# Kernel tuning notes

Hardware: AMD Instinct MI355X
Metric: run time of the kernel (lower is better)

The kernel has to match this reference:

```python
import jax, jax.numpy as jnp
import numpy as np

N = 100000
E = 1600000
IN_DIM = 64
OUT_DIM = 64


def setup_inputs() -> dict:
    key = jax.random.key(0)
    ks = jax.random.split(key, 10)
    q = jax.random.normal(ks[0], (N, IN_DIM), dtype=jnp.float32)
    src1 = jax.random.randint(ks[1], (E,), 0, N, dtype=jnp.int32)
    dst1 = jax.random.randint(ks[2], (E,), 0, N, dtype=jnp.int32)
    src2 = jax.random.randint(ks[3], (E,), 0, N, dtype=jnp.int32)
    dst2 = jax.random.randint(ks[4], (E,), 0, N, dtype=jnp.int32)
    # Learned parameters (torch nn.Linear default-ish init scale)
    s_att = 1.0 / np.sqrt(2 * IN_DIM)
    s_lin = 1.0 / np.sqrt(IN_DIM)
    W_att = jax.random.uniform(ks[5], (2 * IN_DIM,), jnp.float32, -s_att, s_att)  # fc_att weight [1, 2*in_dim] flattened
    W_upd = jax.random.uniform(ks[6], (OUT_DIM, IN_DIM), jnp.float32, -s_lin, s_lin)
    W_V = jax.random.uniform(ks[7], (OUT_DIM, IN_DIM), jnp.float32, -s_lin, s_lin)
    b_V = jax.random.uniform(ks[8], (OUT_DIM,), jnp.float32, -s_lin, s_lin)
    return {"q": q, "W_att": W_att, "W_upd": W_upd, "W_V": W_V, "b_V": b_V,
            "src1": src1, "dst1": dst1, "src2": src2, "dst2": dst2}


def _gat_etype(q, src, dst, W_att, W_V, b_V):
    """One edge-type pass: edge gather -> sigmoid att -> segment softmax over dst -> weighted scatter-sum."""
    d = q.shape[1]
    # fc_att(cat[q_src, q_dst]) == q_src @ W_att[:d] + q_dst @ W_att[d:] (no cat materialized)
    att_src = q @ W_att[:d]           # [N]
    att_dst = q @ W_att[d:]           # [N]
    e = jax.nn.sigmoid(att_src[src] + att_dst[dst])  # [E], in (0,1) so exp is safe without max-shift
    ex = jnp.exp(e)
    denom = jax.ops.segment_sum(ex, dst, num_segments=q.shape[0])  # [N]
    a = ex / jnp.maximum(denom[dst], 1e-12)                        # segment softmax, [E]
    qs = q[src]                                                    # [E, d] edge gather
    OK = jax.ops.segment_sum(a[:, None] * qs, dst, num_segments=q.shape[0])          # [N, d]
    V = qs @ W_V.T + b_V                                                              # [E, out]
    OV = jax.ops.segment_sum(a[:, None] * V, dst, num_segments=q.shape[0])            # [N, out]
    return OK, OV


def reference(q, W_att, W_upd, W_V, b_V, src1, dst1, src2, dst2):
    OK1, OV1 = _gat_etype(q, src1, dst1, W_att, W_V, b_V)
    OK2, OV2 = _gat_etype(q, src2, dst2, W_att, W_V, b_V)
    # multi_update_all cross-reducer 'sum': per-etype reduce (incl. fc_upd) then sum
    q_new = (q + OK1) @ W_upd.T + (q + OK2) @ W_upd.T
    OV = OV1 + OV2
    return q_new, OV
```

## Files before the change

kernel.cpp:

```cpp
#include <hip/hip_runtime.h>
#include <math.h>

#define N_NODES 100000
#define N_EDGES 1600000
#define TWO_E   (2 * N_EDGES)
#define DIM 64
#define SCAN_BLOCKS 98

__device__ __forceinline__ float edge_ex(float as, float ad) {
    float x = as + ad;
    float sg = 1.0f / (1.0f + __expf(-x));
    return __expf(sg);
}

__global__ __launch_bounds__(256) void att_kernel(const float* __restrict__ q,
                                                  const float* __restrict__ W_att,
                                                  float* __restrict__ att_src,
                                                  float* __restrict__ att_dst) {
    int wave = (blockIdx.x * blockDim.x + threadIdx.x) >> 6;
    int lane = threadIdx.x & 63;
    if (wave >= N_NODES) return;
    float qv = q[wave * DIM + lane];
    float ps = qv * W_att[lane];
    float pd = qv * W_att[DIM + lane];
    #pragma unroll
    for (int off = 32; off >= 1; off >>= 1) {
        ps += __shfl_xor(ps, off);
        pd += __shfl_xor(pd, off);
    }
    if (lane == 0) {
        att_src[wave] = ps;
        att_dst[wave] = pd;
    }
}

__global__ __launch_bounds__(256) void hist_kernel(const int* __restrict__ dst1,
                                                   const int* __restrict__ dst2,
                                                   int* __restrict__ count,
                                                   int* __restrict__ rank) {
    int idx = blockIdx.x * blockDim.x + threadIdx.x;
    if (idx >= TWO_E) return;
    int d = (idx < N_EDGES) ? dst1[idx] : dst2[idx - N_EDGES];
    rank[idx] = atomicAdd(count + d, 1);
}

__global__ __launch_bounds__(1024) void scan1_kernel(const int* __restrict__ count,
                                                     int* __restrict__ offsets,
                                                     int* __restrict__ bsum) {
    __shared__ int wtot[16];
    int i = blockIdx.x * 1024 + threadIdx.x;
    int v = (i < N_NODES) ? count[i] : 0;
    int lane = threadIdx.x & 63, wid = threadIdx.x >> 6;
    int x = v;
    #pragma unroll
    for (int off = 1; off <= 32; off <<= 1) {
        int y = __shfl_up(x, off);
        if (lane >= off) x += y;
    }
    if (lane == 63) wtot[wid] = x;
    __syncthreads();
    if (threadIdx.x < 16) {
        int t = wtot[threadIdx.x];
        #pragma unroll
        for (int off = 1; off <= 8; off <<= 1) {
            int y = __shfl_up(t, off);
            if (threadIdx.x >= off) t += y;
        }
        wtot[threadIdx.x] = t;
    }
    __syncthreads();
    int woff = (wid == 0) ? 0 : wtot[wid - 1];
    if (i < N_NODES) offsets[i] = woff + x - v;
    if (threadIdx.x == 0) bsum[blockIdx.x] = wtot[15];
}

__global__ __launch_bounds__(128) void scan2_kernel(const int* __restrict__ bsum,
                                                    int* __restrict__ boff) {
    __shared__ int s[SCAN_BLOCKS];
    if (threadIdx.x < SCAN_BLOCKS) s[threadIdx.x] = bsum[threadIdx.x];
    __syncthreads();
    if (threadIdx.x == 0) {
        int run = 0;
        for (int b = 0; b < SCAN_BLOCKS; ++b) { int t = s[b]; s[b] = run; run += t; }
    }
    __syncthreads();
    if (threadIdx.x < SCAN_BLOCKS) boff[threadIdx.x] = s[threadIdx.x];
}

__global__ __launch_bounds__(1024) void scan3_kernel(int* __restrict__ offsets,
                                                     const int* __restrict__ boff) {
    int i = blockIdx.x * 1024 + threadIdx.x;
    if (i < N_NODES) offsets[i] += boff[blockIdx.x];
    if (i == N_NODES - 1) offsets[N_NODES] = TWO_E;
}

__global__ __launch_bounds__(256) void scatter_kernel(const int* __restrict__ src1, const int* __restrict__ dst1,
                                                      const int* __restrict__ src2, const int* __restrict__ dst2,
                                                      const float* __restrict__ att_src, const float* __restrict__ att_dst,
                                                      const int* __restrict__ offsets, const int* __restrict__ rank,
                                                      uint2* __restrict__ recs) {
    int idx = blockIdx.x * blockDim.x + threadIdx.x;
    if (idx >= TWO_E) return;
    int s, d; unsigned tb;
    if (idx < N_EDGES) { s = src1[idx]; d = dst1[idx]; tb = 0u; }
    else               { s = src2[idx - N_EDGES]; d = dst2[idx - N_EDGES]; tb = 0x80000000u; }
    float ex = edge_ex(att_src[s], att_dst[d]);
    int pos = offsets[d] + rank[idx];
    recs[pos] = make_uint2((unsigned)s | tb, __float_as_uint(ex));
}

__global__ __launch_bounds__(256) void gather_kernel(const float* __restrict__ q,
                                                     const int* __restrict__ offsets,
                                                     const uint2* __restrict__ recs,
                                                     float* __restrict__ S,
                                                     float* __restrict__ fbuf) {
    int node = blockIdx.x * 16 + (threadIdx.x >> 4);
    int t = threadIdx.x & 15;
    if (node >= N_NODES) return;
    int beg = offsets[node], end = offsets[node + 1];
    float d1 = 0.f, d2 = 0.f;
    for (int i = beg + t; i < end; i += 16) {
        uint2 r = recs[i];
        float ex = __uint_as_float(r.y);
        if ((int)r.x < 0) d2 += ex; else d1 += ex;
    }
    #pragma unroll
    for (int off = 8; off >= 1; off >>= 1) {
        d1 += __shfl_xor(d1, off);
        d2 += __shfl_xor(d2, off);
    }
    float inv1 = (d1 > 0.f) ? (1.0f / d1) : 0.f;
    float inv2 = (d2 > 0.f) ? (1.0f / d2) : 0.f;
    if (t == 0) fbuf[node] = ((d1 > 0.f) ? 1.f : 0.f) + ((d2 > 0.f) ? 1.f : 0.f);

    float4 acc = make_float4(0.f, 0.f, 0.f, 0.f);
    const float* qb = q + t * 4;
    int i = beg;
    for (; i + 1 < end; i += 2) {
        uint2 r0 = recs[i], r1 = recs[i + 1];
        int s0 = r0.x & 0x7fffffff, s1 = r1.x & 0x7fffffff;
        float a0 = __uint_as_float(r0.y) * (((int)r0.x < 0) ? inv2 : inv1);
        float a1 = __uint_as_float(r1.y) * (((int)r1.x < 0) ? inv2 : inv1);
        const float4 q0 = *reinterpret_cast<const float4*>(qb + (size_t)s0 * DIM);
        const float4 q1 = *reinterpret_cast<const float4*>(qb + (size_t)s1 * DIM);
        acc.x += a0 * q0.x; acc.y += a0 * q0.y; acc.z += a0 * q0.z; acc.w += a0 * q0.w;
        acc.x += a1 * q1.x; acc.y += a1 * q1.y; acc.z += a1 * q1.z; acc.w += a1 * q1.w;
    }
    if (i < end) {
        uint2 r = recs[i];
        int s = r.x & 0x7fffffff;
        float a = __uint_as_float(r.y) * (((int)r.x < 0) ? inv2 : inv1);
        const float4 qv = *reinterpret_cast<const float4*>(qb + (size_t)s * DIM);
        acc.x += a * qv.x; acc.y += a * qv.y; acc.z += a * qv.z; acc.w += a * qv.w;
    }
    *reinterpret_cast<float4*>(S + (size_t)node * DIM + t * 4) = acc;
}

__global__ __launch_bounds__(512) void final_kernel(const float* __restrict__ q,
                                                    const float* __restrict__ W_upd,
                                                    const float* __restrict__ W_V,
                                                    const float* __restrict__ b_V,
                                                    const float* __restrict__ fbuf,
                                                    float* __restrict__ q_new,
                                                    float* S_and_OV) {
    int lane = threadIdx.x & 63;
    int w = threadIdx.x >> 6;
    int ms = __builtin_amdgcn_readfirstlane(w >> 2);
    int cs = __builtin_amdgcn_readfirstlane(w & 3);
    int node = blockIdx.x * 64 + lane;
    bool active = node < N_NODES;

    float r[DIM];
    float f = 0.f;
    if (active) {
        const float* srow = S_and_OV + (size_t)node * DIM;
        if (ms == 0) {
            #pragma unroll
            for (int k = 0; k < 16; ++k) {
                float4 v = *reinterpret_cast<const float4*>(srow + 4 * k);
                r[4 * k + 0] = v.x; r[4 * k + 1] = v.y;
                r[4 * k + 2] = v.z; r[4 * k + 3] = v.w;
            }
            f = fbuf[node];
        } else {
            const float* qrow = q + (size_t)node * DIM;
            #pragma unroll
            for (int k = 0; k < 16; ++k) {
                float4 sv = *reinterpret_cast<const float4*>(srow + 4 * k);
                float4 qv = *reinterpret_cast<const float4*>(qrow + 4 * k);
                r[4 * k + 0] = 2.f * qv.x + sv.x;
                r[4 * k + 1] = 2.f * qv.y + sv.y;
                r[4 * k + 2] = 2.f * qv.z + sv.z;
                r[4 * k + 3] = 2.f * qv.w + sv.w;
            }
        }
    } else {
        #pragma unroll
        for (int d = 0; d < DIM; ++d) r[d] = 0.f;
    }

    __syncthreads();

    const float* Wbase = ms ? W_upd : W_V;
    float acc[16];
    #pragma unroll
    for (int j = 0; j < 16; ++j) acc[j] = (ms == 0) ? f * b_V[cs * 16 + j] : 0.f;
    #pragma unroll
    for (int j = 0; j < 16; ++j) {
        const float* wr = Wbase + (cs * 16 + j) * DIM;
        float a = acc[j];
        #pragma unroll
        for (int d = 0; d < DIM; ++d) a += r[d] * wr[d];
        acc[j] = a;
    }

    if (active) {
        float* outp = (ms ? q_new : S_and_OV) + (size_t)node * DIM + cs * 16;
        #pragma unroll
        for (int k = 0; k < 4; ++k)
            *reinterpret_cast<float4*>(outp + 4 * k) =
                make_float4(acc[4 * k], acc[4 * k + 1], acc[4 * k + 2], acc[4 * k + 3]);
    }
}

extern "C" void kernel_launch(void* const* d_in, const int* in_sizes, int n_in,
                              void* d_out, int out_size, void* d_ws, size_t ws_size,
                              hipStream_t stream) {
    const float* q     = (const float*)d_in[0];
    const float* W_att = (const float*)d_in[1];
    const float* W_upd = (const float*)d_in[2];
    const float* W_V   = (const float*)d_in[3];
    const float* b_V   = (const float*)d_in[4];
    const int*   src1  = (const int*)d_in[5];
    const int*   dst1  = (const int*)d_in[6];
    const int*   src2  = (const int*)d_in[7];
    const int*   dst2  = (const int*)d_in[8];

    float* out   = (float*)d_out;
    float* q_new = out;
    float* S     = out + (size_t)N_NODES * DIM;
    uint2* recs  = (uint2*)q_new;

    float* att_src = (float*)d_ws;
    float* att_dst = att_src + N_NODES;
    float* fbuf    = att_dst + N_NODES;
    int*   count   = (int*)(fbuf + N_NODES);
    int*   offsets = count + N_NODES;
    int*   bsum    = offsets + N_NODES + 1;
    int*   boff    = bsum + 128;
    int*   rank    = boff + 128;

    hipMemsetAsync(count, 0, (size_t)N_NODES * sizeof(int), stream);

    att_kernel<<<N_NODES / 4, 256, 0, stream>>>(q, W_att, att_src, att_dst);
    hist_kernel<<<(TWO_E + 255) / 256, 256, 0, stream>>>(dst1, dst2, count, rank);
    scan1_kernel<<<SCAN_BLOCKS, 1024, 0, stream>>>(count, offsets, bsum);
    scan2_kernel<<<1, 128, 0, stream>>>(bsum, boff);
    scan3_kernel<<<SCAN_BLOCKS, 1024, 0, stream>>>(offsets, boff);
    scatter_kernel<<<(TWO_E + 255) / 256, 256, 0, stream>>>(
        src1, dst1, src2, dst2, att_src, att_dst, offsets, rank, recs);
    gather_kernel<<<(N_NODES + 15) / 16, 256, 0, stream>>>(q, offsets, recs, S, fbuf);
    final_kernel<<<(N_NODES + 63) / 64, 512, 0, stream>>>(
        q, W_upd, W_V, b_V, fbuf, q_new, S);
}
```

Baseline: 577.2 us.

## Replace per-node CSR sort with coarse 64-node bucket sort and in-LDS regroup

```diff
diff --git a/kernel.cpp b/kernel.cpp
--- a/kernel.cpp
+++ b/kernel.cpp
@@ -5,7 +5,10 @@
 #define N_EDGES 1600000
 #define TWO_E   (2 * N_EDGES)
 #define DIM 64
-#define SCAN_BLOCKS 98
+#define NB 1563
+#define EPB 16384
+#define HS_BLOCKS ((TWO_E + EPB - 1) / EPB)
+#define CAP 2048
 
 __device__ __forceinline__ float edge_ex(float as, float ad) {
     float x = as + ad;
@@ -34,126 +37,168 @@
     }
 }
 
-__global__ __launch_bounds__(256) void hist_kernel(const int* __restrict__ dst1,
-                                                   const int* __restrict__ dst2,
-                                                   int* __restrict__ count,
-                                                   int* __restrict__ rank) {
-    int idx = blockIdx.x * blockDim.x + threadIdx.x;
-    if (idx >= TWO_E) return;
-    int d = (idx < N_EDGES) ? dst1[idx] : dst2[idx - N_EDGES];
-    rank[idx] = atomicAdd(count + d, 1);
-}
-
-__global__ __launch_bounds__(1024) void scan1_kernel(const int* __restrict__ count,
-                                                     int* __restrict__ offsets,
-                                                     int* __restrict__ bsum) {
-    __shared__ int wtot[16];
-    int i = blockIdx.x * 1024 + threadIdx.x;
-    int v = (i < N_NODES) ? count[i] : 0;
-    int lane = threadIdx.x & 63, wid = threadIdx.x >> 6;
-    int x = v;
+__global__ __launch_bounds__(1024) void hist_coarse(const int* __restrict__ dst1,
+                                                    const int* __restrict__ dst2,
+                                                    int* __restrict__ bcount) {
+    __shared__ int lh[NB];
+    for (int b = threadIdx.x; b < NB; b += 1024) lh[b] = 0;
+    __syncthreads();
+    int base = blockIdx.x * EPB;
+    int lim = min(base + EPB, TWO_E);
+    for (int idx = base + threadIdx.x; idx < lim; idx += 1024) {
+        int d = (idx < N_EDGES) ? dst1[idx] : dst2[idx - N_EDGES];
+        atomicAdd(&lh[d >> 6], 1);
+    }
+    __syncthreads();
+    for (int b = threadIdx.x; b < NB; b += 1024)
+        if (lh[b]) atomicAdd(bcount + b, lh[b]);
+}
+
+__global__ __launch_bounds__(1024) void scan_coarse(const int* __restrict__ bcount,
+                                                    int* __restrict__ bbase,
+                                                    int* __restrict__ bcursor) {
+    __shared__ int wt[16];
+    int t = threadIdx.x;
+    int i0 = 2 * t, i1 = 2 * t + 1;
+    int v0 = (i0 < NB) ? bcount[i0] : 0;
+    int v1 = (i1 < NB) ? bcount[i1] : 0;
+    int p = v0 + v1;
+    int lane = t & 63, wid = t >> 6;
+    int x = p;
     #pragma unroll
     for (int off = 1; off <= 32; off <<= 1) {
         int y = __shfl_up(x, off);
         if (lane >= off) x += y;
     }
-    if (lane == 63) wtot[wid] = x;
-    __syncthreads();
-    if (threadIdx.x < 16) {
-        int t = wtot[threadIdx.x];
+    if (lane == 63) wt[wid] = x;
+    __syncthreads();
+    if (t < 16) {
+        int s = wt[t];
         #pragma unroll
         for (int off = 1; off <= 8; off <<= 1) {
-            int y = __shfl_up(t, off);
-            if (threadIdx.x >= off) t += y;
-        }
-        wtot[threadIdx.x] = t;
-    }
-    __syncthreads();
-    int woff = (wid == 0) ? 0 : wtot[wid - 1];
-    if (i < N_NODES) offsets[i] = woff + x - v;
-    if (threadIdx.x == 0) bsum[blockIdx.x] = wtot[15];
-}
-
-__global__ __launch_bounds__(128) void scan2_kernel(const int* __restrict__ bsum,
-                                                    int* __restrict__ boff) {
-    __shared__ int s[SCAN_BLOCKS];
-    if (threadIdx.x < SCAN_BLOCKS) s[threadIdx.x] = bsum[threadIdx.x];
-    __syncthreads();
-    if (threadIdx.x == 0) {
-        int run = 0;
-        for (int b = 0; b < SCAN_BLOCKS; ++b) { int t = s[b]; s[b] = run; run += t; }
-    }
-    __syncthreads();
-    if (threadIdx.x < SCAN_BLOCKS) boff[threadIdx.x] = s[threadIdx.x];
-}
-
-__global__ __launch_bounds__(1024) void scan3_kernel(int* __restrict__ offsets,
-                                                     const int* __restrict__ boff) {
-    int i = blockIdx.x * 1024 + threadIdx.x;
-    if (i < N_NODES) offsets[i] += boff[blockIdx.x];
-    if (i == N_NODES - 1) offsets[N_NODES] = TWO_E;
-}
-
-__global__ __launch_bounds__(256) void scatter_kernel(const int* __restrict__ src1, const int* __restrict__ dst1,
-                                                      const int* __restrict__ src2, const int* __restrict__ dst2,
-                                                      const float* __restrict__ att_src, const float* __restrict__ att_dst,
-                                                      const int* __restrict__ offsets, const int* __restrict__ rank,
-                                                      uint2* __restrict__ recs) {
-    int idx = blockIdx.x * blockDim.x + threadIdx.x;
-    if (idx >= TWO_E) return;
-    int s, d; unsigned tb;
-    if (idx < N_EDGES) { s = src1[idx]; d = dst1[idx]; tb = 0u; }
-    else               { s = src2[idx - N_EDGES]; d = dst2[idx - N_EDGES]; tb = 0x80000000u; }
-    float ex = edge_ex(att_src[s], att_dst[d]);
-    int pos = offsets[d] + rank[idx];
-    recs[pos] = make_uint2((unsigned)s | tb, __float_as_uint(ex));
-}
-
-__global__ __launch_bounds__(256) void gather_kernel(const float* __restrict__ q,
-                                                     const int* __restrict__ offsets,
-                                                     const uint2* __restrict__ recs,
-                                                     float* __restrict__ S,
-                                                     float* __restrict__ fbuf) {
-    int node = blockIdx.x * 16 + (threadIdx.x >> 4);
-    int t = threadIdx.x & 15;
-    if (node >= N_NODES) return;
-    int beg = offsets[node], end = offsets[node + 1];
+            int y = __shfl_up(s, off);
+            if (t >= off) s += y;
+        }
+        wt[t] = s;
+    }
+    __syncthreads();
+    int pre = ((wid ? wt[wid - 1] : 0)) + (x - p);
+    if (i0 < NB) { bbase[i0] = pre;      bcursor[i0] = pre; }
+    if (i1 < NB) { bbase[i1] = pre + v0; bcursor[i1] = pre + v0; }
+    if (t == 0) bbase[NB] = wt[15];
+}
+
+__global__ __launch_bounds__(1024) void scatter_coarse(const int* __restrict__ src1, const int* __restrict__ dst1,
+                                                       const int* __restrict__ src2, const int* __restrict__ dst2,
+                                                       const float* __restrict__ att_src, const float* __restrict__ att_dst,
+                                                       int* __restrict__ bcursor,
+                                                       uint2* __restrict__ recs) {
+    __shared__ int lh[NB];
+    __shared__ int gb[NB];
+    __shared__ int lc[NB];
+    for (int b = threadIdx.x; b < NB; b += 1024) lh[b] = 0;
+    __syncthreads();
+    int base = blockIdx.x * EPB;
+    int lim = min(base + EPB, TWO_E);
+    for (int idx = base + threadIdx.x; idx < lim; idx += 1024) {
+        int d = (idx < N_EDGES) ? dst1[idx] : dst2[idx - N_EDGES];
+        atomicAdd(&lh[d >> 6], 1);
+    }
+    __syncthreads();
+    for (int b = threadIdx.x; b < NB; b += 1024) {
+        int c = lh[b];
+        lc[b] = 0;
+        gb[b] = c ? atomicAdd(bcursor + b, c) : 0;
+    }
+    __syncthreads();
+    for (int idx = base + threadIdx.x; idx < lim; idx += 1024) {
+        int s, d; unsigned ty;
+        if (idx < N_EDGES) { s = src1[idx]; d = dst1[idx]; ty = 0u; }
+        else               { s = src2[idx - N_EDGES]; d = dst2[idx - N_EDGES]; ty = 1u; }
+        int b = d >> 6;
+        int r = atomicAdd(&lc[b], 1);
+        float ex = edge_ex(att_src[s], att_dst[d]);
+        recs[gb[b] + r] = make_uint2((unsigned)s | (ty << 17) | ((unsigned)(d & 63) << 18),
+                                     __float_as_uint(ex));
+    }
+}
+
+__global__ __launch_bounds__(1024) void gather_coarse(const float* __restrict__ q,
+                                                      const int* __restrict__ bbase,
+                                                      const uint2* __restrict__ recs,
+                                                      float* __restrict__ S,
+                                                      float* __restrict__ fbuf) {
+    __shared__ uint2 srt[CAP];
+    __shared__ int cnt[64];
+    __shared__ int cb[64];
+    int tid = threadIdx.x;
+    int bkt = blockIdx.x;
+    int beg = bbase[bkt], end = bbase[bkt + 1];
+    int g = tid >> 4, t16 = tid & 15;
+
+    float4 acc1 = make_float4(0.f, 0.f, 0.f, 0.f);
+    float4 acc2 = make_float4(0.f, 0.f, 0.f, 0.f);
     float d1 = 0.f, d2 = 0.f;
-    for (int i = beg + t; i < end; i += 16) {
-        uint2 r = recs[i];
-        float ex = __uint_as_float(r.y);
-        if ((int)r.x < 0) d2 += ex; else d1 += ex;
-    }
-    #pragma unroll
-    for (int off = 8; off >= 1; off >>= 1) {
-        d1 += __shfl_xor(d1, off);
-        d2 += __shfl_xor(d2, off);
-    }
-    float inv1 = (d1 > 0.f) ? (1.0f / d1) : 0.f;
-    float inv2 = (d2 > 0.f) ? (1.0f / d2) : 0.f;
-    if (t == 0) fbuf[node] = ((d1 > 0.f) ? 1.f : 0.f) + ((d2 > 0.f) ? 1.f : 0.f);
-
-    float4 acc = make_float4(0.f, 0.f, 0.f, 0.f);
-    const float* qb = q + t * 4;
-    int i = beg;
-    for (; i + 1 < end; i += 2) {
-        uint2 r0 = recs[i], r1 = recs[i + 1];
-        int s0 = r0.x & 0x7fffffff, s1 = r1.x & 0x7fffffff;
-        float a0 = __uint_as_float(r0.y) * (((int)r0.x < 0) ? inv2 : inv1);
-        float a1 = __uint_as_float(r1.y) * (((int)r1.x < 0) ? inv2 : inv1);
-        const float4 q0 = *reinterpret_cast<const float4*>(qb + (size_t)s0 * DIM);
-        const float4 q1 = *reinterpret_cast<const float4*>(qb + (size_t)s1 * DIM);
-        acc.x += a0 * q0.x; acc.y += a0 * q0.y; acc.z += a0 * q0.z; acc.w += a0 * q0.w;
-        acc.x += a1 * q1.x; acc.y += a1 * q1.y; acc.z += a1 * q1.z; acc.w += a1 * q1.w;
-    }
-    if (i < end) {
-        uint2 r = recs[i];
-        int s = r.x & 0x7fffffff;
-        float a = __uint_as_float(r.y) * (((int)r.x < 0) ? inv2 : inv1);
-        const float4 qv = *reinterpret_cast<const float4*>(qb + (size_t)s * DIM);
-        acc.x += a * qv.x; acc.y += a * qv.y; acc.z += a * qv.z; acc.w += a * qv.w;
-    }
-    *reinterpret_cast<float4*>(S + (size_t)node * DIM + t * 4) = acc;
+
+    for (int cbeg = beg; cbeg < end; cbeg += CAP) {
+        int C = min(CAP, end - cbeg);
+        __syncthreads();
+        if (tid < 64) cnt[tid] = 0;
+        __syncthreads();
+        uint2 r0, r1; int n0 = -1, n1 = -1, rk0 = 0, rk1 = 0;
+        if (tid < C) {
+            r0 = recs[cbeg + tid];
+            n0 = (r0.x >> 18) & 63;
+            rk0 = atomicAdd(&cnt[n0], 1);
+        }
+        if (tid + 1024 < C) {
+            r1 = recs[cbeg + tid + 1024];
+            n1 = (r1.x >> 18) & 63;
+            rk1 = atomicAdd(&cnt[n1], 1);
+        }
+        __syncthreads();
+        if (tid < 64) {
+            int c = cnt[tid];
+            int incl = c;
+            #pragma unroll
+            for (int off = 1; off <= 32; off <<= 1) {
+                int y = __shfl_up(incl, off);
+                if (tid >= off) incl += y;
+            }
+            cb[tid] = incl - c;
+        }
+        __syncthreads();
+        if (n0 >= 0) srt[cb[n0] + rk0] = r0;
+        if (n1 >= 0) srt[cb[n1] + rk1] = r1;
+        __syncthreads();
+        int s0 = cb[g], e0 = s0 + cnt[g];
+        for (int k = s0; k < e0; ++k) {
+            uint2 r = srt[k];
+            int s = r.x & 0x1FFFF;
+            float exv = __uint_as_float(r.y);
+            int ty = (r.x >> 17) & 1;
+            float w1 = ty ? 0.f : exv;
+            float w2 = ty ? exv : 0.f;
+            d1 += w1; d2 += w2;
+            const float4 qv = *reinterpret_cast<const float4*>(q + (size_t)s * DIM + t16 * 4);
+            acc1.x += w1 * qv.x; acc1.y += w1 * qv.y; acc1.z += w1 * qv.z; acc1.w += w1 * qv.w;
+            acc2.x += w2 * qv.x; acc2.y += w2 * qv.y; acc2.z += w2 * qv.z; acc2.w += w2 * qv.w;
+        }
+    }
+
+    float inv1 = (d1 > 0.f) ? 1.0f / d1 : 0.f;
+    float inv2 = (d2 > 0.f) ? 1.0f / d2 : 0.f;
+    int node = bkt * 64 + g;
+    if (node < N_NODES) {
+        float4 sv;
+        sv.x = acc1.x * inv1 + acc2.x * inv2;
+        sv.y = acc1.y * inv1 + acc2.y * inv2;
+        sv.z = acc1.z * inv1 + acc2.z * inv2;
+        sv.w = acc1.w * inv1 + acc2.w * inv2;
+        *reinterpret_cast<float4*>(S + (size_t)node * DIM + t16 * 4) = sv;
+        if (t16 == 0)
+            fbuf[node] = ((d1 > 0.f) ? 1.f : 0.f) + ((d2 > 0.f) ? 1.f : 0.f);
+    }
 }
 
 __global__ __launch_bounds__(512) void final_kernel(const float* __restrict__ q,
@@ -244,22 +289,18 @@
     float* att_src = (float*)d_ws;
     float* att_dst = att_src + N_NODES;
     float* fbuf    = att_dst + N_NODES;
-    int*   count   = (int*)(fbuf + N_NODES);
-    int*   offsets = count + N_NODES;
-    int*   bsum    = offsets + N_NODES + 1;
-    int*   boff    = bsum + 128;
-    int*   rank    = boff + 128;
-
-    hipMemsetAsync(count, 0, (size_t)N_NODES * sizeof(int), stream);
+    int*   bcount  = (int*)(fbuf + N_NODES);
+    int*   bbase   = bcount + NB;
+    int*   bcursor = bbase + NB + 1;
+
+    hipMemsetAsync(bcount, 0, NB * sizeof(int), stream);
 
     att_kernel<<<N_NODES / 4, 256, 0, stream>>>(q, W_att, att_src, att_dst);
-    hist_kernel<<<(TWO_E + 255) / 256, 256, 0, stream>>>(dst1, dst2, count, rank);
-    scan1_kernel<<<SCAN_BLOCKS, 1024, 0, stream>>>(count, offsets, bsum);
-    scan2_kernel<<<1, 128, 0, stream>>>(bsum, boff);
-    scan3_kernel<<<SCAN_BLOCKS, 1024, 0, stream>>>(offsets, boff);
-    scatter_kernel<<<(TWO_E + 255) / 256, 256, 0, stream>>>(
-        src1, dst1, src2, dst2, att_src, att_dst, offsets, rank, recs);
-    gather_kernel<<<(N_NODES + 15) / 16, 256, 0, stream>>>(q, offsets, recs, S, fbuf);
+    hist_coarse<<<HS_BLOCKS, 1024, 0, stream>>>(dst1, dst2, bcount);
+    scan_coarse<<<1, 1024, 0, stream>>>(bcount, bbase, bcursor);
+    scatter_coarse<<<HS_BLOCKS, 1024, 0, stream>>>(
+        src1, dst1, src2, dst2, att_src, att_dst, bcursor, recs);
+    gather_coarse<<<NB, 1024, 0, stream>>>(q, bbase, recs, S, fbuf);
     final_kernel<<<(N_NODES + 63) / 64, 512, 0, stream>>>(
         q, W_upd, W_V, b_V, fbuf, q_new, S);
 }
```

Result: faster. 463.7 us (-19.7%).
